# Kernel tuning notes

Hardware: AMD Instinct MI355X
Metric: run time of the kernel (lower is better)

## Reference

```python
import jax, jax.numpy as jnp
import numpy as np

B, J = 1000000, 17

def setup_inputs() -> dict:
    key = jax.random.key(0)
    k1, k2, k3 = jax.random.split(key, 3)
    output = jax.random.uniform(k1, (B, J, 3), dtype=jnp.float32)  # class channel in (0,1) for BCE
    reg_gt = jax.random.uniform(k2, (B, J, 2), dtype=jnp.float32)
    class_gt = (jax.random.uniform(k3, (B, J)) > 0.5).astype(jnp.float32)  # binary {0,1}
    target = jnp.concatenate([reg_gt, class_gt[:, :, None]], axis=2)
    return {"output": output, "target": target}

def reference(output, target):
    reg_pred = output[:, :, :2]          # [B,J,2]
    class_pred = output[:, :, 2]         # [B,J]
    reg_gt = target[:, :, :2]
    class_gt = target[:, :, 2]

    # nn.BCELoss (mean reduction), with torch's log clamp at -100
    log_p = jnp.maximum(jnp.log(class_pred), -100.0)
    log_1mp = jnp.maximum(jnp.log1p(-class_pred), -100.0)
    loss_class = -jnp.mean(class_gt * log_p + (1.0 - class_gt) * log_1mp)

    # masked_fill(mask < 0.5, 0) on BOTH pred and gt -> masked entries contribute 0 to MSE sum
    keep = class_pred[:, :, None] >= 0.5                       # [B,J,1] broadcast over 2 coords
    diff = jnp.where(keep, reg_pred - reg_gt, 0.0)             # [B,J,2]
    sq_sum = jnp.sum(diff * diff, axis=(1, 2))                 # [B]

    # per-batch joint count: 1 + #(class_gt == 1)
    num_joints = 1.0 + jnp.sum((class_gt == 1.0).astype(diff.dtype), axis=1)  # [B]

    loss_reg = jnp.mean(0.5 * sq_sum / num_joints)  # == (sum over batch)/batch_size
    return loss_class + loss_reg
```

## Files before the change

### kernel.cpp

```cpp
#include <hip/hip_runtime.h>
#include <hip/hip_bf16.h>
#include <stdint.h>

#define J_JOINTS 17
#define ROW_F 51
#define BLOCK 256
#define TILE_ROWS 64
#define TILE_F (TILE_ROWS * ROW_F)
#define TILE_CHUNKS (TILE_F / 4)
#define GRID 768

__device__ __forceinline__ void gld_lds16(const float* g, float* l) {
    __builtin_amdgcn_global_load_lds(
        (const __attribute__((address_space(1))) void*)g,
        (__attribute__((address_space(3))) void*)l,
        16, 0, 0);
}

__global__ __launch_bounds__(BLOCK) void loss_main_kernel(
    const float* __restrict__ outp,
    const float* __restrict__ tgt,
    double* __restrict__ acc,
    int B)
{
    __shared__ float so[2][TILE_F];
    __shared__ float st[2][TILE_F];

    const int tid = threadIdx.x;
    const int r4  = tid >> 2;
    const int q   = tid & 3;

    float cls_acc = 0.0f;
    float reg_acc = 0.0f;

    const int tiles_total = (B + TILE_ROWS - 1) / TILE_ROWS;

    auto stage_async = [&](int row0, int buf) {
        const float* go = outp + row0 * ROW_F;
        const float* gt = tgt  + row0 * ROW_F;
        float* lo = so[buf];
        float* lt = st[buf];
        #pragma unroll
        for (int j = 0; j < 4; ++j) {
            const int i = tid + j * BLOCK;
            if (i < TILE_CHUNKS) {
                gld_lds16(go + i * 4, lo + i * 4);
                gld_lds16(gt + i * 4, lt + i * 4);
            }
        }
    };
    auto stage_sync = [&](int row0, int rows_valid, int buf) {
        const float* go = outp + row0 * ROW_F;
        const float* gt = tgt  + row0 * ROW_F;
        const int nv = rows_valid * ROW_F;
        const int n4 = nv >> 2;
        for (int i = tid; i < n4; i += BLOCK) {
            reinterpret_cast<float4*>(so[buf])[i] = reinterpret_cast<const float4*>(go)[i];
            reinterpret_cast<float4*>(st[buf])[i] = reinterpret_cast<const float4*>(gt)[i];
        }
        const int tb = n4 << 2;
        if (tid < nv - tb) {
            so[buf][tb + tid] = go[tb + tid];
            st[buf][tb + tid] = gt[tb + tid];
        }
    };
    auto stage = [&](int tk, int buf) {
        const int row0 = tk * TILE_ROWS;
        if (row0 + TILE_ROWS <= B) stage_async(row0, buf);
        else                       stage_sync(row0, B - row0, buf);
    };

    int tk  = blockIdx.x;
    int cur = 0;

    if (tk < tiles_total) stage(tk, 0);
    asm volatile("s_waitcnt vmcnt(0)" ::: "memory");
    __syncthreads();

    while (tk < tiles_total) {
        const int tn = tk + GRID;
        if (tn < tiles_total) stage(tn, cur ^ 1);

        const int rows_valid = min(TILE_ROWS, B - tk * TILE_ROWS);
        float sq = 0.0f;
        float nj = 0.0f;
        if (r4 < rows_valid) {
            const float* lo = so[cur] + r4 * ROW_F + q * 12;
            const float* lt = st[cur] + r4 * ROW_F + q * 12;
            #pragma unroll
            for (int k = 0; k < 4; ++k) {
                const float ox = lo[3*k + 0];
                const float oy = lo[3*k + 1];
                const float oz = lo[3*k + 2];
                const float tx = lt[3*k + 0];
                const float ty = lt[3*k + 1];
                const float tz = lt[3*k + 2];

                const bool gt1 = (tz == 1.0f);
                cls_acc += fmaxf(__logf(gt1 ? oz : (1.0f - oz)), -100.0f);

                const bool keep = (oz >= 0.5f);
                const float d0 = keep ? (ox - tx) : 0.0f;
                const float d1 = keep ? (oy - ty) : 0.0f;
                sq = fmaf(d0, d0, fmaf(d1, d1, sq));
                nj += gt1 ? 1.0f : 0.0f;
            }
            if (q == 3) {
                const float ox = lo[12 + 0];
                const float oy = lo[12 + 1];
                const float oz = lo[12 + 2];
                const float tx = lt[12 + 0];
                const float ty = lt[12 + 1];
                const float tz = lt[12 + 2];

                const bool gt1 = (tz == 1.0f);
                cls_acc += fmaxf(__logf(gt1 ? oz : (1.0f - oz)), -100.0f);

                const bool keep = (oz >= 0.5f);
                const float d0 = keep ? (ox - tx) : 0.0f;
                const float d1 = keep ? (oy - ty) : 0.0f;
                sq = fmaf(d0, d0, fmaf(d1, d1, sq));
                nj += gt1 ? 1.0f : 0.0f;
            }
        }
        sq += __shfl_xor(sq, 1, 64);  nj += __shfl_xor(nj, 1, 64);
        sq += __shfl_xor(sq, 2, 64);  nj += __shfl_xor(nj, 2, 64);
        if (q == 0 && r4 < rows_valid) {
            reg_acc += __fdividef(0.5f * sq, 1.0f + nj);
        }

        asm volatile("s_waitcnt vmcnt(0)" ::: "memory");
        __syncthreads();
        cur ^= 1;
        tk = tn;
    }

    #pragma unroll
    for (int m = 1; m < 64; m <<= 1) {
        cls_acc += __shfl_xor(cls_acc, m, 64);
        reg_acc += __shfl_xor(reg_acc, m, 64);
    }
    __shared__ float s_cls[BLOCK / 64];
    __shared__ float s_reg[BLOCK / 64];
    const int wid = tid >> 6;
    if ((tid & 63) == 0) {
        s_cls[wid] = cls_acc;
        s_reg[wid] = reg_acc;
    }
    __syncthreads();
    if (tid == 0) {
        float c = 0.0f, r = 0.0f;
        #pragma unroll
        for (int w = 0; w < BLOCK / 64; ++w) { c += s_cls[w]; r += s_reg[w]; }
        atomicAdd(&acc[0], (double)c);
        atomicAdd(&acc[1], (double)r);
    }
}

__global__ void loss_finalize_kernel(const double* __restrict__ acc,
                                     float* __restrict__ out, int B)
{
    const double cls_sum = acc[0];
    const double reg_sum = acc[1];
    const double loss_class = -cls_sum / ((double)B * (double)J_JOINTS);
    const double loss_reg   = reg_sum / (double)B;
    out[0] = (float)(loss_class + loss_reg);
}

extern "C" void kernel_launch(void* const* d_in, const int* in_sizes, int n_in,
                              void* d_out, int out_size, void* d_ws, size_t ws_size,
                              hipStream_t stream) {
    const float* outp = (const float*)d_in[0];
    const float* tgt  = (const float*)d_in[1];
    float* out = (float*)d_out;
    const int B = in_sizes[0] / (J_JOINTS * 3);

    double* acc = (double*)d_ws;
    hipMemsetAsync(acc, 0, 2 * sizeof(double), stream);

    loss_main_kernel<<<GRID, BLOCK, 0, stream>>>(outp, tgt, acc, B);
    loss_finalize_kernel<<<1, 1, 0, stream>>>(acc, out, B);
}
```

Baseline: 87.49 us.

## Read output tensor directly from global memory, stage only target in LDS, double grid

The output tensor is no longer staged into shared memory through async global-to-LDS loads. Each thread now reads its 12-float span straight from global memory with 3-float struct loads, while the target keeps the double-buffered LDS path. Halving shared memory per block allows more resident blocks, and the grid is doubled to 1536. The direct reads lose the 16-byte async coalescing and are not overlapped with compute the way the prefetched target is, so global access efficiency may drop.

```diff
diff --git a/kernel.cpp b/kernel.cpp
--- a/kernel.cpp
+++ b/kernel.cpp
@@ -8,7 +8,9 @@
 #define TILE_ROWS 64
 #define TILE_F (TILE_ROWS * ROW_F)
 #define TILE_CHUNKS (TILE_F / 4)
-#define GRID 768
+#define GRID 1536
+
+struct __align__(4) F3 { float x, y, z; };
 
 __device__ __forceinline__ void gld_lds16(const float* g, float* l) {
     __builtin_amdgcn_global_load_lds(
@@ -23,10 +25,11 @@
     double* __restrict__ acc,
     int B)
 {
-    __shared__ float so[2][TILE_F];
     __shared__ float st[2][TILE_F];
 
     const int tid = threadIdx.x;
+    const int wv  = tid >> 6;
+    const int ln  = tid & 63;
     const int r4  = tid >> 2;
     const int q   = tid & 3;
 
@@ -36,31 +39,25 @@
     const int tiles_total = (B + TILE_ROWS - 1) / TILE_ROWS;
 
     auto stage_async = [&](int row0, int buf) {
-        const float* go = outp + row0 * ROW_F;
-        const float* gt = tgt  + row0 * ROW_F;
-        float* lo = so[buf];
+        const float* gt = tgt + row0 * ROW_F;
         float* lt = st[buf];
         #pragma unroll
         for (int j = 0; j < 4; ++j) {
             const int i = tid + j * BLOCK;
             if (i < TILE_CHUNKS) {
-                gld_lds16(go + i * 4, lo + i * 4);
                 gld_lds16(gt + i * 4, lt + i * 4);
             }
         }
     };
     auto stage_sync = [&](int row0, int rows_valid, int buf) {
-        const float* go = outp + row0 * ROW_F;
-        const float* gt = tgt  + row0 * ROW_F;
+        const float* gt = tgt + row0 * ROW_F;
         const int nv = rows_valid * ROW_F;
         const int n4 = nv >> 2;
         for (int i = tid; i < n4; i += BLOCK) {
-            reinterpret_cast<float4*>(so[buf])[i] = reinterpret_cast<const float4*>(go)[i];
             reinterpret_cast<float4*>(st[buf])[i] = reinterpret_cast<const float4*>(gt)[i];
         }
         const int tb = n4 << 2;
         if (tid < nv - tb) {
-            so[buf][tb + tid] = go[tb + tid];
             st[buf][tb + tid] = gt[tb + tid];
         }
     };
@@ -85,40 +82,37 @@
         float sq = 0.0f;
         float nj = 0.0f;
         if (r4 < rows_valid) {
-            const float* lo = so[cur] + r4 * ROW_F + q * 12;
-            const float* lt = st[cur] + r4 * ROW_F + q * 12;
+            const int row_g = tk * TILE_ROWS + r4;
+            const float* po = outp + row_g * ROW_F + q * 12;
+            const float* lt = &st[cur][r4 * ROW_F + q * 12];
             #pragma unroll
             for (int k = 0; k < 4; ++k) {
-                const float ox = lo[3*k + 0];
-                const float oy = lo[3*k + 1];
-                const float oz = lo[3*k + 2];
+                const F3 o = *reinterpret_cast<const F3*>(po + 3 * k);
                 const float tx = lt[3*k + 0];
                 const float ty = lt[3*k + 1];
                 const float tz = lt[3*k + 2];
 
                 const bool gt1 = (tz == 1.0f);
-                cls_acc += fmaxf(__logf(gt1 ? oz : (1.0f - oz)), -100.0f);
+                cls_acc += fmaxf(__logf(gt1 ? o.z : (1.0f - o.z)), -100.0f);
 
-                const bool keep = (oz >= 0.5f);
-                const float d0 = keep ? (ox - tx) : 0.0f;
-                const float d1 = keep ? (oy - ty) : 0.0f;
+                const bool keep = (o.z >= 0.5f);
+                const float d0 = keep ? (o.x - tx) : 0.0f;
+                const float d1 = keep ? (o.y - ty) : 0.0f;
                 sq = fmaf(d0, d0, fmaf(d1, d1, sq));
                 nj += gt1 ? 1.0f : 0.0f;
             }
             if (q == 3) {
-                const float ox = lo[12 + 0];
-                const float oy = lo[12 + 1];
-                const float oz = lo[12 + 2];
+                const F3 o = *reinterpret_cast<const F3*>(po + 12);
                 const float tx = lt[12 + 0];
                 const float ty = lt[12 + 1];
                 const float tz = lt[12 + 2];
 
                 const bool gt1 = (tz == 1.0f);
-                cls_acc += fmaxf(__logf(gt1 ? oz : (1.0f - oz)), -100.0f);
+                cls_acc += fmaxf(__logf(gt1 ? o.z : (1.0f - o.z)), -100.0f);
 
-                const bool keep = (oz >= 0.5f);
-                const float d0 = keep ? (ox - tx) : 0.0f;
-                const float d1 = keep ? (oy - ty) : 0.0f;
+                const bool keep = (o.z >= 0.5f);
+                const float d0 = keep ? (o.x - tx) : 0.0f;
+                const float d1 = keep ? (o.y - ty) : 0.0f;
                 sq = fmaf(d0, d0, fmaf(d1, d1, sq));
                 nj += gt1 ? 1.0f : 0.0f;
             }
@@ -142,10 +136,9 @@
     }
     __shared__ float s_cls[BLOCK / 64];
     __shared__ float s_reg[BLOCK / 64];
-    const int wid = tid >> 6;
-    if ((tid & 63) == 0) {
-        s_cls[wid] = cls_acc;
-        s_reg[wid] = reg_acc;
+    if (ln == 0) {
+        s_cls[wv] = cls_acc;
+        s_reg[wv] = reg_acc;
     }
     __syncthreads();
     if (tid == 0) {
```

Measured after the change: 98.65 us. 12.8% more time.
